# Kernel tuning notes

Hardware: AMD Instinct MI355X
Metric: run time of the kernel (lower is better)

The kernel has to match this reference:

```python
import jax, jax.numpy as jnp
import numpy as np

N = 100000   # nodes
E = 1600000  # edges
G = 512      # graphs in batch
F_IN = 30
H = 128
EPS = 1e-5   # BatchNorm1d default eps


def setup_inputs() -> dict:
    key = jax.random.key(0)
    ks = jax.random.split(key, 16)
    x = jax.random.normal(ks[0], (N, F_IN), dtype=jnp.float32)
    edge_index = jax.random.randint(ks[1], (2, E), 0, N, dtype=jnp.int64)
    batch = jnp.sort(jax.random.randint(ks[2], (N,), 0, G, dtype=jnp.int64))
    d = {"x": x, "edge_index": edge_index, "batch": batch}
    dims = [(F_IN, H), (H, H), (H, H)]
    for i, (din, dout) in enumerate(dims):
        d[f"W{i}"] = jax.random.normal(ks[3 + i], (din, dout), dtype=jnp.float32) * (1.0 / np.sqrt(din))
        d[f"b{i}"] = jnp.zeros((dout,), dtype=jnp.float32)
        d[f"g{i}"] = jnp.ones((dout,), dtype=jnp.float32)   # BN gamma
        d[f"bt{i}"] = jnp.zeros((dout,), dtype=jnp.float32)  # BN beta
    d["HW1"] = jax.random.normal(ks[9], (H, 64), dtype=jnp.float32) * (1.0 / np.sqrt(H))
    d["Hb1"] = jnp.zeros((64,), dtype=jnp.float32)
    d["HW2"] = jax.random.normal(ks[10], (64, 1), dtype=jnp.float32) * 0.125
    d["Hb2"] = jnp.zeros((1,), dtype=jnp.float32)
    return d


def _bn(x, gamma, beta):
    # training-mode BatchNorm1d over node dim, biased variance (as torch uses for normalization)
    mu = jnp.mean(x, axis=0)
    var = jnp.mean(jnp.square(x - mu), axis=0)
    return (x - mu) * jax.lax.rsqrt(var + EPS) * gamma + beta


def reference(x, edge_index, batch, W0, b0, g0, bt0, W1, b1, g1, bt1, W2, b2, g2, bt2, HW1, Hb1, HW2, Hb2):
    # GCNConv: add self-loops, symmetric D^{-1/2}(A+I)D^{-1/2} normalization
    loop = jnp.arange(N, dtype=edge_index.dtype)
    src = jnp.concatenate([edge_index[0], loop])  # [E+N]
    dst = jnp.concatenate([edge_index[1], loop])
    deg = jax.ops.segment_sum(jnp.ones(src.shape, jnp.float32), dst, num_segments=N)
    dinv = jax.lax.rsqrt(jnp.maximum(deg, 1.0))  # deg >= 1 due to self-loops
    norm = (dinv[src] * dinv[dst])[:, None]      # [E+N, 1]

    for W, b, g, bt in ((W0, b0, g0, bt0), (W1, b1, g1, bt1), (W2, b2, g2, bt2)):
        h = x @ W                                           # [N, H]
        agg = jax.ops.segment_sum(h[src] * norm, dst, num_segments=N) + b
        x = jnp.maximum(_bn(agg, g, bt), 0.0)               # BN + ReLU (dropout = identity here)

    # global_mean_pool over graph ids
    counts = jax.ops.segment_sum(jnp.ones((N,), jnp.float32), batch, num_segments=G)
    pooled = jax.ops.segment_sum(x, batch, num_segments=G) / jnp.maximum(counts, 1.0)[:, None]

    h = jnp.maximum(pooled @ HW1 + Hb1, 0.0)
    return (h @ HW2 + Hb2).squeeze(-1)  # [G]
```

## Files before the change

### kernel.cpp

```cpp
#include <hip/hip_runtime.h>

#define BN_EPS 1e-5f
#define BSH 8

typedef __attribute__((ext_vector_type(8))) short bf16x8;
typedef __attribute__((ext_vector_type(4))) float f32x4;

__device__ inline float bfhi(unsigned int v) { return __uint_as_float(v & 0xFFFF0000u); }
__device__ inline float bflo(unsigned int v) { return __uint_as_float(v << 16); }
__device__ inline unsigned short f2bf(float f) {
  unsigned int u = __float_as_uint(f);
  u += 0x7FFFu + ((u >> 16) & 1u);
  return (unsigned short)(u >> 16);
}
__device__ inline unsigned int pack2bf(float lo, float hi) {
  return (unsigned int)f2bf(lo) | ((unsigned int)f2bf(hi) << 16);
}

__global__ void k_bucket(const int* __restrict__ src, const int* __restrict__ dst,
                         int* __restrict__ gcur, uint2* __restrict__ sedge,
                         int NB, int CAP, int E) {
  __shared__ int lh[512], rb[512];
  int tid = threadIdx.x;
  for (int i = tid; i < NB; i += 256) lh[i] = 0;
  __syncthreads();
  int base = blockIdx.x * 8192;
  int lim = min(8192, E - base);
  for (int i = tid; i < lim; i += 256)
    atomicAdd(&lh[dst[base + i] >> BSH], 1);
  __syncthreads();
  for (int i = tid; i < NB; i += 256) {
    int c = lh[i];
    rb[i] = c ? atomicAdd(&gcur[i], c) : 0;
    lh[i] = 0;
  }
  __syncthreads();
  for (int i = tid; i < lim; i += 256) {
    int d = dst[base + i];
    int s = src[base + i];
    int b = d >> BSH;
    int pos = rb[b] + atomicAdd(&lh[b], 1);
    if (pos < CAP) {
      uint2 v; v.x = (unsigned int)s; v.y = (unsigned int)d;
      sedge[(size_t)b * CAP + pos] = v;
    }
  }
}

__global__ void k_csr1(const uint2* __restrict__ sedge, const int* __restrict__ gcur,
                       int* __restrict__ startv, int* __restrict__ cnt,
                       float* __restrict__ dinv, int CAP, int n) {
  int b = blockIdx.x, tid = threadIdx.x;
  __shared__ int h[256], sc[256];
  h[tid] = 0;
  __syncthreads();
  int cb = gcur[b]; if (cb > CAP) cb = CAP;
  const uint2* sd = sedge + (size_t)b * CAP;
  for (int i = tid; i < cb; i += 256) atomicAdd(&h[sd[i].y & 255], 1);
  __syncthreads();
  int v = h[tid];
  sc[tid] = v;
  __syncthreads();
  for (int o = 1; o < 256; o <<= 1) {
    int t = (tid >= o) ? sc[tid - o] : 0;
    __syncthreads();
    sc[tid] += t;
    __syncthreads();
  }
  int gd = (b << BSH) + tid;
  if (gd < n) {
    startv[gd] = b * CAP + (sc[tid] - v);
    cnt[gd] = v;
    dinv[gd] = rsqrtf((float)v + 1.0f);
  }
}

__global__ void k_csr2(const uint2* __restrict__ sedge, const int* __restrict__ gcur,
                       const int* __restrict__ startv, const float* __restrict__ dinv,
                       unsigned int* __restrict__ elist, int CAP, int n) {
  int b = blockIdx.x, tid = threadIdx.x;
  __shared__ int cur[256];
  int gd = (b << BSH) + tid;
  cur[tid] = (gd < n) ? startv[gd] : 0;
  __syncthreads();
  int cb = gcur[b]; if (cb > CAP) cb = CAP;
  const uint2* sd = sedge + (size_t)b * CAP;
  for (int i = tid; i < cb; i += 256) {
    uint2 e = sd[i];
    int pos = atomicAdd(&cur[e.y & 255], 1);
    unsigned int u = (unsigned int)(dinv[e.x] * 32767.0f + 0.5f);
    elist[pos] = e.x | (u << 17);
  }
}

__global__ void k_cvtall(const float* __restrict__ x, const float* __restrict__ W0,
                         const float* __restrict__ W1, const float* __restrict__ W2,
                         unsigned short* __restrict__ xb, unsigned short* __restrict__ Wt0,
                         unsigned short* __restrict__ Wt1, unsigned short* __restrict__ Wt2,
                         int n) {
  int t = blockIdx.x * blockDim.x + threadIdx.x;
  if (t < 4096) {
    int nn = t >> 5, k = t & 31;
    Wt0[t] = f2bf(k < 30 ? W0[k * 128 + nn] : 0.f);
  } else if (t < 20480) {
    int i = t - 4096; int nn = i >> 7, k = i & 127;
    Wt1[i] = f2bf(W1[k * 128 + nn]);
  } else if (t < 36864) {
    int i = t - 20480; int nn = i >> 7, k = i & 127;
    Wt2[i] = f2bf(W2[k * 128 + nn]);
  } else {
    int i = t - 36864;
    if (i < n * 32) {
      int row = i >> 5, c = i & 31;
      xb[i] = f2bf(c < 30 ? x[row * 30 + c] : 0.f);
    }
  }
}

__global__ void k_gather0(const unsigned int* __restrict__ elist, const int* __restrict__ start,
                          const int* __restrict__ cnt, const float* __restrict__ dinv,
                          const uint4* __restrict__ x4,
                          unsigned int* __restrict__ G0, int n) {
  int lane = threadIdx.x & 63;
  int wv   = threadIdx.x >> 6;
  int grp  = lane >> 2;
  int q4   = lane & 3;
  int row  = blockIdx.x * 4 + wv;
  bool active = row < n;

  float acc[8];
  float di = 0.f, dq = 0.f;
  int len = 0;
  const unsigned int* ep = elist;
  if (active) {
    di = dinv[row];
    dq = di * (1.0f / 32767.0f);
    len = cnt[row];
    ep = elist + start[row];
  }
  {
    float selfw = (grp == 0 && active) ? di * di : 0.f;
    uint4 hv = (grp == 0 && active) ? x4[(size_t)row * 4 + q4] : make_uint4(0, 0, 0, 0);
    acc[0] = bflo(hv.x) * selfw; acc[1] = bfhi(hv.x) * selfw;
    acc[2] = bflo(hv.y) * selfw; acc[3] = bfhi(hv.y) * selfw;
    acc[4] = bflo(hv.z) * selfw; acc[5] = bfhi(hv.z) * selfw;
    acc[6] = bflo(hv.w) * selfw; acc[7] = bfhi(hv.w) * selfw;
  }
  for (int j = 0; j < len; j += 16) {
    int jj = j + grp;
    unsigned int e = (jj < len) ? ep[jj] : 0u;
    uint4 v = x4[(size_t)(e & 0x1FFFFu) * 4 + q4];
    float w = (float)(e >> 17) * dq;
    acc[0] = fmaf(bflo(v.x), w, acc[0]); acc[1] = fmaf(bfhi(v.x), w, acc[1]);
    acc[2] = fmaf(bflo(v.y), w, acc[2]); acc[3] = fmaf(bfhi(v.y), w, acc[3]);
    acc[4] = fmaf(bflo(v.z), w, acc[4]); acc[5] = fmaf(bfhi(v.z), w, acc[5]);
    acc[6] = fmaf(bflo(v.w), w, acc[6]); acc[7] = fmaf(bfhi(v.w), w, acc[7]);
  }
#pragma unroll
  for (int k = 0; k < 8; ++k) {
    acc[k] += __shfl_xor(acc[k], 4);
    acc[k] += __shfl_xor(acc[k], 8);
    acc[k] += __shfl_xor(acc[k], 16);
    acc[k] += __shfl_xor(acc[k], 32);
  }
  if (grp == 0 && active) {
    uint4 o;
    o.x = pack2bf(acc[0], acc[1]);
    o.y = pack2bf(acc[2], acc[3]);
    o.z = pack2bf(acc[4], acc[5]);
    o.w = pack2bf(acc[6], acc[7]);
    ((uint4*)G0)[(size_t)row * 4 + q4] = o;
  }
}

__global__ void k_gemm_mfma(const unsigned short* __restrict__ A,
                            const unsigned short* __restrict__ Wt,
                            const float* __restrict__ scsh, int doBN,
                            const float* __restrict__ bias, float* __restrict__ bnslab,
                            int doStats, unsigned short* __restrict__ C, int n, int Kp) {
  __shared__ float ssc[128], ssh[128];
  if (doBN) {
    if (threadIdx.x < 128) {
      ssc[threadIdx.x] = scsh[threadIdx.x];
      ssh[threadIdx.x] = scsh[128 + threadIdx.x];
    }
    __syncthreads();
  }
  int wave = threadIdx.x >> 6;
  int lane = threadIdx.x & 63;
  int m0 = blockIdx.x * 128 + wave * 32;
  int lm = lane & 15;
  int lq = lane >> 4;

  f32x4 acc[2][8] = {};
  const unsigned short* Arow0 = A + (size_t)(m0 + lm) * Kp + lq * 8;
  const unsigned short* Arow1 = Arow0 + (size_t)16 * Kp;
  const unsigned short* Bbase = Wt + (size_t)lm * Kp + lq * 8;

  for (int k0 = 0; k0 < Kp; k0 += 32) {
    uint4 ra0 = *(const uint4*)(Arow0 + k0);
    uint4 ra1 = *(const uint4*)(Arow1 + k0);
    bf16x8 a0, a1;
    if (doBN) {
      int cb = k0 + lq * 8;
      unsigned int w0 = pack2bf(fmaxf(fmaf(bflo(ra0.x), ssc[cb+0], ssh[cb+0]), 0.f),
                                fmaxf(fmaf(bfhi(ra0.x), ssc[cb+1], ssh[cb+1]), 0.f));
      unsigned int w1 = pack2bf(fmaxf(fmaf(bflo(ra0.y), ssc[cb+2], ssh[cb+2]), 0.f),
                                fmaxf(fmaf(bfhi(ra0.y), ssc[cb+3], ssh[cb+3]), 0.f));
      unsigned int w2 = pack2bf(fmaxf(fmaf(bflo(ra0.z), ssc[cb+4], ssh[cb+4]), 0.f),
                                fmaxf(fmaf(bfhi(ra0.z), ssc[cb+5], ssh[cb+5]), 0.f));
      unsigned int w3 = pack2bf(fmaxf(fmaf(bflo(ra0.w), ssc[cb+6], ssh[cb+6]), 0.f),
                                fmaxf(fmaf(bfhi(ra0.w), ssc[cb+7], ssh[cb+7]), 0.f));
      uint4 pa0 = make_uint4(w0, w1, w2, w3);
      a0 = *(bf16x8*)&pa0;
      unsigned int y0 = pack2bf(fmaxf(fmaf(bflo(ra1.x), ssc[cb+0], ssh[cb+0]), 0.f),
                                fmaxf(fmaf(bfhi(ra1.x), ssc[cb+1], ssh[cb+1]), 0.f));
      unsigned int y1 = pack2bf(fmaxf(fmaf(bflo(ra1.y), ssc[cb+2], ssh[cb+2]), 0.f),
                                fmaxf(fmaf(bfhi(ra1.y), ssc[cb+3], ssh[cb+3]), 0.f));
      unsigned int y2 = pack2bf(fmaxf(fmaf(bflo(ra1.z), ssc[cb+4], ssh[cb+4]), 0.f),
                                fmaxf(fmaf(bfhi(ra1.z), ssc[cb+5], ssh[cb+5]), 0.f));
      unsigned int y3 = pack2bf(fmaxf(fmaf(bflo(ra1.w), ssc[cb+6], ssh[cb+6]), 0.f),
                                fmaxf(fmaf(bfhi(ra1.w), ssc[cb+7], ssh[cb+7]), 0.f));
      uint4 pa1 = make_uint4(y0, y1, y2, y3);
      a1 = *(bf16x8*)&pa1;
    } else {
      a0 = *(bf16x8*)&ra0;
      a1 = *(bf16x8*)&ra1;
    }
#pragma unroll
    for (int t = 0; t < 8; ++t) {
      bf16x8 b = *(const bf16x8*)(Bbase + (size_t)t * 16 * Kp + k0);
      acc[0][t] = __builtin_amdgcn_mfma_f32_16x16x32_bf16(a0, b, acc[0][t], 0, 0, 0);
      acc[1][t] = __builtin_amdgcn_mfma_f32_16x16x32_bf16(a1, b, acc[1][t], 0, 0, 0);
    }
  }

#pragma unroll
  for (int h = 0; h < 2; ++h) {
    int rbase = m0 + h * 16 + lq * 4;
#pragma unroll
    for (int t = 0; t < 8; ++t) {
      int col = t * 16 + lm;
      float bv = doStats ? bias[col] : 0.f;
#pragma unroll
      for (int r = 0; r < 4; ++r) {
        int row = rbase + r;
        if (row < n) C[(size_t)row * 128 + col] = f2bf(acc[h][t][r] + bv);
      }
    }
  }

  if (doStats) {
    __shared__ float sms[4][256];
#pragma unroll
    for (int t = 0; t < 8; ++t) {
      int col = t * 16 + lm;
      float bv = bias[col];
      float s = 0.f, s2 = 0.f;
#pragma unroll
      for (int h = 0; h < 2; ++h) {
        int rbase = m0 + h * 16 + lq * 4;
#pragma unroll
        for (int r = 0; r < 4; ++r) {
          if (rbase + r < n) {
            float v = acc[h][t][r] + bv;
            s += v; s2 = fmaf(v, v, s2);
          }
        }
      }
      s  += __shfl_xor(s, 16);  s  += __shfl_xor(s, 32);
      s2 += __shfl_xor(s2, 16); s2 += __shfl_xor(s2, 32);
      if (lq == 0) { sms[wave][col] = s; sms[wave][128 + col] = s2; }
    }
    __syncthreads();
    int tid = threadIdx.x;
    int slab = (blockIdx.x & 63) * 256;
    float tot = sms[0][tid] + sms[1][tid] + sms[2][tid] + sms[3][tid];
    atomicAdd(&bnslab[slab + tid], tot);
  }
}

__global__ void k_gather(const unsigned int* __restrict__ elist, const int* __restrict__ start,
                         const int* __restrict__ cnt, const float* __restrict__ dinv,
                         const uint4* __restrict__ h4,
                         const float* __restrict__ bias, unsigned int* __restrict__ agg,
                         float* __restrict__ bnsumP, int n) {
  int lane = threadIdx.x & 63;
  int wv   = threadIdx.x >> 6;
  int grp  = lane >> 4;
  int c8   = lane & 15;
  int row  = blockIdx.x * 4 + wv;
  bool active = row < n;

  float acc[8];
  float di = 0.f, dq = 0.f;
  int len = 0;
  const unsigned int* ep = elist;

  if (active) {
    di = dinv[row];
    dq = di * (1.0f / 32767.0f);
    len = cnt[row];
    ep = elist + start[row];
  }

  {
    float selfw = (grp == 0 && active) ? di * di : 0.f;
    float4 b0 = make_float4(0.f, 0.f, 0.f, 0.f), b1 = b0;
    if (grp == 0 && active) {
      b0 = ((const float4*)bias)[c8 * 2];
      b1 = ((const float4*)bias)[c8 * 2 + 1];
    }
    uint4 hv = active ? h4[(size_t)row * 16 + c8] : make_uint4(0, 0, 0, 0);
    acc[0] = fmaf(bflo(hv.x), selfw, b0.x);
    acc[1] = fmaf(bfhi(hv.x), selfw, b0.y);
    acc[2] = fmaf(bflo(hv.y), selfw, b0.z);
    acc[3] = fmaf(bfhi(hv.y), selfw, b0.w);
    acc[4] = fmaf(bflo(hv.z), selfw, b1.x);
    acc[5] = fmaf(bfhi(hv.z), selfw, b1.y);
    acc[6] = fmaf(bflo(hv.w), selfw, b1.z);
    acc[7] = fmaf(bfhi(hv.w), selfw, b1.w);
  }

  int j = 0;
  for (; j + 8 <= len; j += 8) {
    unsigned int e0 = ep[j + grp];
    unsigned int e1 = ep[j + 4 + grp];
    uint4 v0 = h4[(size_t)(e0 & 0x1FFFFu) * 16 + c8];
    uint4 v1 = h4[(size_t)(e1 & 0x1FFFFu) * 16 + c8];
    float w0 = (float)(e0 >> 17) * dq;
    float w1 = (float)(e1 >> 17) * dq;
    acc[0] = fmaf(bflo(v0.x), w0, acc[0]); acc[1] = fmaf(bfhi(v0.x), w0, acc[1]);
    acc[2] = fmaf(bflo(v0.y), w0, acc[2]); acc[3] = fmaf(bfhi(v0.y), w0, acc[3]);
    acc[4] = fmaf(bflo(v0.z), w0, acc[4]); acc[5] = fmaf(bfhi(v0.z), w0, acc[5]);
    acc[6] = fmaf(bflo(v0.w), w0, acc[6]); acc[7] = fmaf(bfhi(v0.w), w0, acc[7]);
    acc[0] = fmaf(bflo(v1.x), w1, acc[0]); acc[1] = fmaf(bfhi(v1.x), w1, acc[1]);
    acc[2] = fmaf(bflo(v1.y), w1, acc[2]); acc[3] = fmaf(bfhi(v1.y), w1, acc[3]);
    acc[4] = fmaf(bflo(v1.z), w1, acc[4]); acc[5] = fmaf(bfhi(v1.z), w1, acc[5]);
    acc[6] = fmaf(bflo(v1.w), w1, acc[6]); acc[7] = fmaf(bfhi(v1.w), w1, acc[7]);
  }
  for (; j < len; j += 4) {
    int jj = j + grp;
    unsigned int e = (jj < len) ? ep[jj] : 0u;
    uint4 v = h4[(size_t)(e & 0x1FFFFu) * 16 + c8];
    float w = (float)(e >> 17) * dq;
    acc[0] = fmaf(bflo(v.x), w, acc[0]); acc[1] = fmaf(bfhi(v.x), w, acc[1]);
    acc[2] = fmaf(bflo(v.y), w, acc[2]); acc[3] = fmaf(bfhi(v.y), w, acc[3]);
    acc[4] = fmaf(bflo(v.z), w, acc[4]); acc[5] = fmaf(bfhi(v.z), w, acc[5]);
    acc[6] = fmaf(bflo(v.w), w, acc[6]); acc[7] = fmaf(bfhi(v.w), w, acc[7]);
  }

#pragma unroll
  for (int k = 0; k < 8; ++k) {
    acc[k] += __shfl_xor(acc[k], 16);
    acc[k] += __shfl_xor(acc[k], 32);
  }

  __shared__ float sm[2][4][128];
  if (lane < 16) {
    if (active) {
      uint4 o;
      o.x = pack2bf(acc[0], acc[1]);
      o.y = pack2bf(acc[2], acc[3]);
      o.z = pack2bf(acc[4], acc[5]);
      o.w = pack2bf(acc[6], acc[7]);
      ((uint4*)agg)[(size_t)row * 16 + c8] = o;
    }
#pragma unroll
    for (int k = 0; k < 8; ++k) {
      float a = acc[k];
      sm[0][wv][c8 * 8 + k] = a;
      sm[1][wv][c8 * 8 + k] = a * a;
    }
  }
  __syncthreads();
  int tid = threadIdx.x;
  int slab = (blockIdx.x & 63) * 256;
  if (tid < 128) {
    float s = sm[0][0][tid] + sm[0][1][tid] + sm[0][2][tid] + sm[0][3][tid];
    atomicAdd(&bnsumP[slab + tid], s);
  } else {
    int c = tid - 128;
    float s = sm[1][0][c] + sm[1][1][c] + sm[1][2][c] + sm[1][3][c];
    atomicAdd(&bnsumP[slab + 128 + c], s);
  }
}

__global__ void k_bnfinal(const float* __restrict__ bnsumP, const float* __restrict__ gamma,
                          const float* __restrict__ beta, float* __restrict__ scsh, int n) {
  int c = threadIdx.x;
  float s = 0.f, s2 = 0.f;
  for (int k = 0; k < 64; ++k) {
    s  += bnsumP[k * 256 + c];
    s2 += bnsumP[k * 256 + 128 + c];
  }
  float invn = 1.0f / (float)n;
  float mu  = s * invn;
  float ex2 = s2 * invn;
  float var = fmaxf(ex2 - mu * mu, 0.f);
  float sc = gamma[c] * rsqrtf(var + BN_EPS);
  scsh[c] = sc;
  scsh[128 + c] = fmaf(-mu, sc, beta[c]);
}

__global__ void k_poolhead(const unsigned int* __restrict__ aggd, const float* __restrict__ scsh,
                           const int* __restrict__ batch, const float* __restrict__ HW1,
                           const float* __restrict__ Hb1, const float* __restrict__ HW2,
                           const float* __restrict__ Hb2, float* __restrict__ out, int n) {
  int g = blockIdx.x;
  int wv = threadIdx.x >> 6, t = threadIdx.x & 63;
  int lo = 0, hi = n;
  while (lo < hi) { int mid = (lo + hi) >> 1; if (batch[mid] < g) lo = mid + 1; else hi = mid; }
  int s = lo;
  lo = 0; hi = n;
  int g1 = g + 1;
  while (lo < hi) { int mid = (lo + hi) >> 1; if (batch[mid] < g1) lo = mid + 1; else hi = mid; }
  int e = lo;

  float sc0 = scsh[2 * t], sc1 = scsh[2 * t + 1];
  float sh0 = scsh[128 + 2 * t], sh1 = scsh[128 + 2 * t + 1];
  float a0 = 0.f, a1 = 0.f;
  for (int i = s + wv; i < e; i += 4) {
    unsigned int u = aggd[(size_t)i * 64 + t];
    a0 += fmaxf(fmaf(bflo(u), sc0, sh0), 0.f);
    a1 += fmaxf(fmaf(bfhi(u), sc1, sh1), 0.f);
  }
  __shared__ float pp[4][128];
  pp[wv][2 * t] = a0;
  pp[wv][2 * t + 1] = a1;
  __syncthreads();
  if (wv == 0) {
    float inv = 1.0f / fmaxf((float)(e - s), 1.f);
    float p0 = (pp[0][2 * t] + pp[1][2 * t] + pp[2][2 * t] + pp[3][2 * t]) * inv;
    float p1 = (pp[0][2 * t + 1] + pp[1][2 * t + 1] + pp[2][2 * t + 1] + pp[3][2 * t + 1]) * inv;
    pp[0][2 * t] = p0;
    pp[0][2 * t + 1] = p1;
    float acc = Hb1[t];
    for (int k = 0; k < 128; ++k) acc = fmaf(pp[0][k], HW1[k * 64 + t], acc);
    float v = fmaxf(acc, 0.f) * HW2[t];
    for (int off = 32; off > 0; off >>= 1) v += __shfl_down(v, off);
    if (t == 0) out[g] = v + Hb2[0];
  }
}

extern "C" void kernel_launch(void* const* d_in, const int* in_sizes, int n_in,
                              void* d_out, int out_size, void* d_ws, size_t ws_size,
                              hipStream_t stream) {
  const int F_IN = 30, H = 128;
  const float* x   = (const float*)d_in[0];
  const int* eidx  = (const int*)d_in[1];
  const int* batch = (const int*)d_in[2];
  const int N = in_sizes[0] / F_IN;
  const int E = in_sizes[1] / 2;
  const int G = out_size;
  const int* srcp = eidx;
  const int* dstp = eidx + E;
  const float* HW1 = (const float*)d_in[15];
  const float* Hb1 = (const float*)d_in[16];
  const float* HW2 = (const float*)d_in[17];
  const float* Hb2 = (const float*)d_in[18];
  float* outp = (float*)d_out;

  const int Npad = (N + 127) & ~127;
  size_t nh = (size_t)Npad * H;
  const int NB = (N + 255) >> BSH;
  const int CAP = ((E / NB) * 3) / 2 + 128;
  const int NBpad = (NB + 63) & ~63;

  unsigned short* bufH = (unsigned short*)d_ws;
  unsigned short* bufX = bufH + nh;
  unsigned short* xbf  = bufX + nh;
  unsigned short* G0   = xbf + (size_t)Npad * 32;
  float* dinv = (float*)(G0 + (size_t)Npad * 32);
  int*   cnt    = (int*)(dinv + N);
  int*   startv = cnt + N;
  int*   gcur   = startv + N;
  float* bnsumP = (float*)(gcur + NBpad);
  float* scsh   = bnsumP + 3 * 64 * 256;
  unsigned short* Wt0 = (unsigned short*)(scsh + 256);
  unsigned short* Wt1 = Wt0 + 128 * 32;
  unsigned short* Wt2 = Wt1 + 128 * 128;
  unsigned int* elist = (unsigned int*)(Wt2 + 128 * 128 + 64);
  uint2* sedge = (uint2*)bufX;

  hipMemsetAsync(gcur, 0, ((size_t)NBpad + 3 * 64 * 256) * sizeof(int), stream);

  k_bucket<<<(E + 8191) / 8192, 256, 0, stream>>>(srcp, dstp, gcur, sedge, NB, CAP, E);
  k_csr1<<<NB, 256, 0, stream>>>(sedge, gcur, startv, cnt, dinv, CAP, N);
  k_csr2<<<NB, 256, 0, stream>>>(sedge, gcur, startv, dinv, elist, CAP, N);

  k_cvtall<<<(36864 + N * 32 + 255) / 256, 256, 0, stream>>>(
      x, (const float*)d_in[3], (const float*)d_in[7], (const float*)d_in[11],
      xbf, Wt0, Wt1, Wt2, N);

  const float* b0  = (const float*)d_in[4];
  const float* gm0 = (const float*)d_in[5];
  const float* bt0 = (const float*)d_in[6];

  k_gather0<<<(N + 3) / 4, 256, 0, stream>>>(elist, startv, cnt, dinv,
                                             (const uint4*)xbf, (unsigned int*)G0, N);
  k_gemm_mfma<<<Npad / 128, 256, 0, stream>>>(G0, Wt0, scsh, 0, b0, bnsumP, 1,
                                              bufX, N, 32);
  k_bnfinal<<<1, 128, 0, stream>>>(bnsumP, gm0, bt0, scsh, N);

  const unsigned short* Wts[3] = {nullptr, Wt1, Wt2};
  for (int l = 1; l < 3; ++l) {
    const float* b  = (const float*)d_in[4 + l * 4];
    const float* gm = (const float*)d_in[5 + l * 4];
    const float* bt = (const float*)d_in[6 + l * 4];
    float* bnslab = bnsumP + (size_t)l * 64 * 256;

    k_gemm_mfma<<<Npad / 128, 256, 0, stream>>>(bufX, Wts[l], scsh, 1, nullptr, nullptr, 0,
                                                bufH, N, 128);
    k_gather<<<(N + 3) / 4, 256, 0, stream>>>(elist, startv, cnt, dinv,
                                              (const uint4*)bufH, b,
                                              (unsigned int*)bufX, bnslab, N);
    k_bnfinal<<<1, 128, 0, stream>>>(bnslab, gm, bt, scsh, N);
  }

  k_poolhead<<<G, 256, 0, stream>>>((const unsigned int*)bufX, scsh, batch,
                                    HW1, Hb1, HW2, Hb2, outp, N);
}
```

Before: 461.6 us.

## Split gather feature columns across two blocks and parallelize BN finalize

The layer gather kernel now launches twice as many blocks. Each block handles one 64-column half of each row, so a wave processes 8 edges at a time with 8 lanes per edge instead of 4 edges with 16 lanes. This raises parallelism and the number of gathers in flight per row. The cost is reading the edge list twice and doing an extra shuffle-reduction step. The BN finalize kernel also uses 256 threads, summing the sum and sum-of-squares slabs in parallel before combining them in shared memory.

```diff
diff --git a/kernel.cpp b/kernel.cpp
--- a/kernel.cpp
+++ b/kernel.cpp
@@ -287,16 +287,18 @@
                          float* __restrict__ bnsumP, int n) {
   int lane = threadIdx.x & 63;
   int wv   = threadIdx.x >> 6;
-  int grp  = lane >> 4;
-  int c8   = lane & 15;
-  int row  = blockIdx.x * 4 + wv;
+  int half = blockIdx.x & 1;
+  int blk  = blockIdx.x >> 1;
+  int grp  = lane >> 3;
+  int c    = lane & 7;
+  int hc   = half * 8 + c;
+  int row  = blk * 4 + wv;
   bool active = row < n;
 
   float acc[8];
   float di = 0.f, dq = 0.f;
   int len = 0;
   const unsigned int* ep = elist;
-
   if (active) {
     di = dinv[row];
     dq = di * (1.0f / 32767.0f);
@@ -308,10 +310,10 @@
     float selfw = (grp == 0 && active) ? di * di : 0.f;
     float4 b0 = make_float4(0.f, 0.f, 0.f, 0.f), b1 = b0;
     if (grp == 0 && active) {
-      b0 = ((const float4*)bias)[c8 * 2];
-      b1 = ((const float4*)bias)[c8 * 2 + 1];
-    }
-    uint4 hv = active ? h4[(size_t)row * 16 + c8] : make_uint4(0, 0, 0, 0);
+      b0 = ((const float4*)bias)[hc * 2];
+      b1 = ((const float4*)bias)[hc * 2 + 1];
+    }
+    uint4 hv = (grp == 0 && active) ? h4[(size_t)row * 16 + hc] : make_uint4(0, 0, 0, 0);
     acc[0] = fmaf(bflo(hv.x), selfw, b0.x);
     acc[1] = fmaf(bfhi(hv.x), selfw, b0.y);
     acc[2] = fmaf(bflo(hv.y), selfw, b0.z);
@@ -323,11 +325,11 @@
   }
 
   int j = 0;
-  for (; j + 8 <= len; j += 8) {
+  for (; j + 16 <= len; j += 16) {
     unsigned int e0 = ep[j + grp];
-    unsigned int e1 = ep[j + 4 + grp];
-    uint4 v0 = h4[(size_t)(e0 & 0x1FFFFu) * 16 + c8];
-    uint4 v1 = h4[(size_t)(e1 & 0x1FFFFu) * 16 + c8];
+    unsigned int e1 = ep[j + 8 + grp];
+    uint4 v0 = h4[(size_t)(e0 & 0x1FFFFu) * 16 + hc];
+    uint4 v1 = h4[(size_t)(e1 & 0x1FFFFu) * 16 + hc];
     float w0 = (float)(e0 >> 17) * dq;
     float w1 = (float)(e1 >> 17) * dq;
     acc[0] = fmaf(bflo(v0.x), w0, acc[0]); acc[1] = fmaf(bfhi(v0.x), w0, acc[1]);
@@ -339,10 +341,10 @@
     acc[4] = fmaf(bflo(v1.z), w1, acc[4]); acc[5] = fmaf(bfhi(v1.z), w1, acc[5]);
     acc[6] = fmaf(bflo(v1.w), w1, acc[6]); acc[7] = fmaf(bfhi(v1.w), w1, acc[7]);
   }
-  for (; j < len; j += 4) {
+  for (; j < len; j += 8) {
     int jj = j + grp;
     unsigned int e = (jj < len) ? ep[jj] : 0u;
-    uint4 v = h4[(size_t)(e & 0x1FFFFu) * 16 + c8];
+    uint4 v = h4[(size_t)(e & 0x1FFFFu) * 16 + hc];
     float w = (float)(e >> 17) * dq;
     acc[0] = fmaf(bflo(v.x), w, acc[0]); acc[1] = fmaf(bfhi(v.x), w, acc[1]);
     acc[2] = fmaf(bflo(v.y), w, acc[2]); acc[3] = fmaf(bfhi(v.y), w, acc[3]);
@@ -352,55 +354,60 @@
 
 #pragma unroll
   for (int k = 0; k < 8; ++k) {
+    acc[k] += __shfl_xor(acc[k], 8);
     acc[k] += __shfl_xor(acc[k], 16);
     acc[k] += __shfl_xor(acc[k], 32);
   }
 
-  __shared__ float sm[2][4][128];
-  if (lane < 16) {
+  __shared__ float sm[2][4][64];
+  if (grp == 0) {
     if (active) {
       uint4 o;
       o.x = pack2bf(acc[0], acc[1]);
       o.y = pack2bf(acc[2], acc[3]);
       o.z = pack2bf(acc[4], acc[5]);
       o.w = pack2bf(acc[6], acc[7]);
-      ((uint4*)agg)[(size_t)row * 16 + c8] = o;
+      ((uint4*)agg)[(size_t)row * 16 + hc] = o;
     }
 #pragma unroll
     for (int k = 0; k < 8; ++k) {
       float a = acc[k];
-      sm[0][wv][c8 * 8 + k] = a;
-      sm[1][wv][c8 * 8 + k] = a * a;
+      sm[0][wv][c * 8 + k] = a;
+      sm[1][wv][c * 8 + k] = a * a;
     }
   }
   __syncthreads();
   int tid = threadIdx.x;
-  int slab = (blockIdx.x & 63) * 256;
-  if (tid < 128) {
+  int slab = (blk & 63) * 256;
+  if (tid < 64) {
     float s = sm[0][0][tid] + sm[0][1][tid] + sm[0][2][tid] + sm[0][3][tid];
-    atomicAdd(&bnsumP[slab + tid], s);
-  } else {
-    int c = tid - 128;
-    float s = sm[1][0][c] + sm[1][1][c] + sm[1][2][c] + sm[1][3][c];
-    atomicAdd(&bnsumP[slab + 128 + c], s);
+    atomicAdd(&bnsumP[slab + half * 64 + tid], s);
+  } else if (tid < 128) {
+    int cc = tid - 64;
+    float s2 = sm[1][0][cc] + sm[1][1][cc] + sm[1][2][cc] + sm[1][3][cc];
+    atomicAdd(&bnsumP[slab + 128 + half * 64 + cc], s2);
   }
 }
 
 __global__ void k_bnfinal(const float* __restrict__ bnsumP, const float* __restrict__ gamma,
                           const float* __restrict__ beta, float* __restrict__ scsh, int n) {
-  int c = threadIdx.x;
-  float s = 0.f, s2 = 0.f;
-  for (int k = 0; k < 64; ++k) {
-    s  += bnsumP[k * 256 + c];
-    s2 += bnsumP[k * 256 + 128 + c];
-  }
-  float invn = 1.0f / (float)n;
-  float mu  = s * invn;
-  float ex2 = s2 * invn;
-  float var = fmaxf(ex2 - mu * mu, 0.f);
-  float sc = gamma[c] * rsqrtf(var + BN_EPS);
-  scsh[c] = sc;
-  scsh[128 + c] = fmaf(-mu, sc, beta[c]);
+  int tid = threadIdx.x;
+  int c = tid & 127;
+  int which = tid >> 7;
+  float s = 0.f;
+  for (int k = 0; k < 64; ++k) s += bnsumP[k * 256 + which * 128 + c];
+  __shared__ float sh[256];
+  sh[tid] = s;
+  __syncthreads();
+  if (tid < 128) {
+    float invn = 1.0f / (float)n;
+    float mu  = sh[tid] * invn;
+    float ex2 = sh[128 + tid] * invn;
+    float var = fmaxf(ex2 - mu * mu, 0.f);
+    float sc = gamma[tid] * rsqrtf(var + BN_EPS);
+    scsh[tid] = sc;
+    scsh[128 + tid] = fmaf(-mu, sc, beta[tid]);
+  }
 }
 
 __global__ void k_poolhead(const unsigned int* __restrict__ aggd, const float* __restrict__ scsh,
@@ -501,7 +508,7 @@
                                              (const uint4*)xbf, (unsigned int*)G0, N);
   k_gemm_mfma<<<Npad / 128, 256, 0, stream>>>(G0, Wt0, scsh, 0, b0, bnsumP, 1,
                                               bufX, N, 32);
-  k_bnfinal<<<1, 128, 0, stream>>>(bnsumP, gm0, bt0, scsh, N);
+  k_bnfinal<<<1, 256, 0, stream>>>(bnsumP, gm0, bt0, scsh, N);
 
   const unsigned short* Wts[3] = {nullptr, Wt1, Wt2};
   for (int l = 1; l < 3; ++l) {
@@ -512,10 +519,10 @@
 
     k_gemm_mfma<<<Npad / 128, 256, 0, stream>>>(bufX, Wts[l], scsh, 1, nullptr, nullptr, 0,
                                                 bufH, N, 128);
-    k_gather<<<(N + 3) / 4, 256, 0, stream>>>(elist, startv, cnt, dinv,
-                                              (const uint4*)bufH, b,
-                                              (unsigned int*)bufX, bnslab, N);
-    k_bnfinal<<<1, 128, 0, stream>>>(bnslab, gm, bt, scsh, N);
+    k_gather<<<2 * ((N + 3) / 4), 256, 0, stream>>>(elist, startv, cnt, dinv,
+                                                    (const uint4*)bufH, b,
+                                                    (unsigned int*)bufX, bnslab, N);
+    k_bnfinal<<<1, 256, 0, stream>>>(bnslab, gm, bt, scsh, N);
   }
 
   k_poolhead<<<G, 256, 0, stream>>>((const unsigned int*)bufX, scsh, batch,
```

Result: slower. 505.2 us (+9.4%).
